# Kernel optimization log

Hardware: AMD Instinct MI355X
Metric: run time of the kernel (lower is better)

The kernel has to match this reference:

```python
import jax, jax.numpy as jnp
import numpy as np

N, E, G, L, D = 50000, 800000, 512, 3, 128
BN_EPS = 1e-5


def setup_inputs() -> dict:
    key = jax.random.key(0)
    ks = jax.random.split(key, 16)
    x = jax.random.normal(ks[0], (N, D), dtype=jnp.float32)
    edge_index = jax.random.randint(ks[1], (2, E), 0, N)
    batch = jnp.sort(jax.random.randint(ks[2], (N,), 0, G))
    W1 = jax.random.normal(ks[3], (L, D, D), dtype=jnp.float32) * 0.05
    b1 = jax.random.normal(ks[4], (L, D), dtype=jnp.float32) * 0.05
    gamma = jax.random.uniform(ks[5], (L, D), dtype=jnp.float32) + 0.5
    beta = jax.random.normal(ks[6], (L, D), dtype=jnp.float32) * 0.05
    running_mean = jax.random.normal(ks[7], (L, D), dtype=jnp.float32) * 0.1
    running_var = jax.random.uniform(ks[8], (L, D), dtype=jnp.float32) + 0.5
    W2 = jax.random.normal(ks[9], (L, D, D), dtype=jnp.float32) * 0.05
    b2 = jax.random.normal(ks[10], (L, D), dtype=jnp.float32) * 0.05
    lin1_W = jax.random.normal(ks[11], (L * D, L * D), dtype=jnp.float32) * 0.05
    lin1_b = jax.random.normal(ks[12], (L * D,), dtype=jnp.float32) * 0.05
    lin2_W = jax.random.normal(ks[13], (L * D, 10), dtype=jnp.float32) * 0.05
    lin2_b = jax.random.normal(ks[14], (10,), dtype=jnp.float32) * 0.05
    return {"x": x, "edge_index": edge_index, "batch": batch,
            "W1": W1, "b1": b1, "gamma": gamma, "beta": beta,
            "running_mean": running_mean, "running_var": running_var,
            "W2": W2, "b2": b2, "lin1_W": lin1_W, "lin1_b": lin1_b,
            "lin2_W": lin2_W, "lin2_b": lin2_b}


def _gin_layer(h, src, dst, W1, b1, gamma, beta, rm, rv, W2, b2):
    # GINConv (eps=0): MLP((1+eps)*x + sum_{j->i} x_j); aggregate src->dst
    agg = jax.ops.segment_sum(h[src], dst, num_segments=N)  # [N, D]
    z = (h + agg) @ W1 + b1
    # BatchNorm1d in eval mode (running stats)
    z = (z - rm) * (gamma / jnp.sqrt(rv + BN_EPS)) + beta
    z = jax.nn.relu(z)
    return jax.nn.relu(z @ W2 + b2)


def reference(x, edge_index, batch, W1, b1, gamma, beta, running_mean,
              running_var, W2, b2, lin1_W, lin1_b, lin2_W, lin2_b):
    src, dst = edge_index[0], edge_index[1]
    h = x
    pooled = []
    for i in range(L):
        h = _gin_layer(h, src, dst, W1[i], b1[i], gamma[i], beta[i],
                       running_mean[i], running_var[i], W2[i], b2[i])
        pooled.append(jax.ops.segment_sum(h, batch, num_segments=G))  # [G, D]
    g = jnp.concatenate(pooled, axis=1)  # [G, L*D]
    g = jax.nn.relu(g @ lin1_W + lin1_b)
    # dropout is identity in eval mode
    return g @ lin2_W + lin2_b  # [G, num_classes]
```

## Files before the change

### kernel.cpp

```cpp
#include <hip/hip_runtime.h>
#include <hip/hip_bf16.h>

#define D_FEAT 128
#define N_GRAPHS 512
#define N_LAYERS 3
#define POOL_DIM (N_LAYERS * D_FEAT)
#define N_CLASSES 10
#define BN_EPS 1e-5f
#define CAP 64
#define NBINS 8
#define SLABCAP 768


typedef __attribute__((ext_vector_type(8))) short bf16x8;
typedef __attribute__((ext_vector_type(8))) unsigned short ushort8;
typedef __attribute__((ext_vector_type(4))) float f32x4;

__device__ __forceinline__ unsigned short f2bf(float f) {
    unsigned u = __builtin_bit_cast(unsigned, f);
    u += 0x7FFFu + ((u >> 16) & 1u);
    return (unsigned short)(u >> 16);
}
__device__ __forceinline__ float bf2f(unsigned short h) {
    unsigned u = ((unsigned)h) << 16;
    return __builtin_bit_cast(float, u);
}
__device__ __forceinline__ float bf_lo(unsigned u) {
    return __builtin_bit_cast(float, u << 16);
}
__device__ __forceinline__ float bf_hi(unsigned u) {
    return __builtin_bit_cast(float, u & 0xffff0000u);
}

__global__ __launch_bounds__(256) void setup_kernel(
        const float* __restrict__ x, unsigned short* __restrict__ xb,
        const float* __restrict__ W1, const float* __restrict__ W2,
        unsigned short* __restrict__ Wt,
        const float* __restrict__ b1, const float* __restrict__ gamma,
        const float* __restrict__ beta, const float* __restrict__ rm,
        const float* __restrict__ rv, const float* __restrict__ b2,
        float* __restrict__ ea, float* __restrict__ eb,
        int* __restrict__ cursor, float* __restrict__ pooled,
        const int* __restrict__ ei, int2* __restrict__ pairs,
        int* __restrict__ cnts, int E,
        int N, int n4, int B0, int B1, int B2, int B3, int B4) {
    int b = blockIdx.x, tid = threadIdx.x;
    if (b < B0) {
        int i = b * 256 + tid;
        if (i < n4) {
            float4 v = ((const float4*)x)[i];
            ushort4 o;
            o.x = f2bf(v.x); o.y = f2bf(v.y); o.z = f2bf(v.z); o.w = f2bf(v.w);
            ((ushort4*)xb)[i] = o;
        }
    } else if (b < B1) {
        __shared__ float tile[64][65];
        int t = b - B0;
        int slot = t >> 2;
        int r0 = ((t >> 1) & 1) * 64;
        int c0 = (t & 1) * 64;
        int l = slot >> 1;
        const float* W = (slot & 1) ? W2 : W1;
        const float* Wb = W + (size_t)l * D_FEAT * D_FEAT;
        int rr = tid >> 2, cc4 = (tid & 3) * 16;
        #pragma unroll
        for (int j = 0; j < 16; ++j)
            tile[rr][cc4 + j] = Wb[(size_t)(r0 + rr) * D_FEAT + c0 + cc4 + j];
        __syncthreads();
        int nn = tid >> 2, kk4 = (tid & 3) * 16;
        unsigned short* Wo = Wt + (size_t)slot * D_FEAT * D_FEAT;
        #pragma unroll
        for (int j = 0; j < 16; ++j)
            Wo[(size_t)(c0 + nn) * D_FEAT + r0 + kk4 + j] = f2bf(tile[kk4 + j][nn]);
    } else if (b < B2) {
        int i = (b - B1) * 256 + tid;
        if (i < N_LAYERS * D_FEAT) {
            int l = i >> 7, c = i & 127;
            float s = gamma[i] * rsqrtf(rv[i] + BN_EPS);
            ea[(2 * l) * D_FEAT + c] = s;
            eb[(2 * l) * D_FEAT + c] = (b1[i] - rm[i]) * s + beta[i];
            ea[(2 * l + 1) * D_FEAT + c] = 1.0f;
            eb[(2 * l + 1) * D_FEAT + c] = b2[i];
        }
    } else if (b < B3) {
        int i = (b - B2) * 256 + tid;
        if (i < N) cursor[i] = 0;
    } else if (b < B4) {
        int i = (b - B3) * 256 + tid;
        if (i < N_GRAPHS * POOL_DIM) pooled[i] = 0.f;
    } else {
        __shared__ int loc[NBINS];
        int bb = b - B4;
        int per = (E + 255) / 256;
        int e0 = bb * per;
        int e1 = e0 + per; if (e1 > E) e1 = E;
        int span = (N + NBINS - 1) / NBINS;
        if (tid < NBINS) loc[tid] = 0;
        __syncthreads();
        for (int e = e0 + tid; e < e1; e += 256) {
            int dst = ei[E + e];
            int src = ei[e];
            int bin = dst / span;
            int p = atomicAdd(&loc[bin], 1);
            if (p < SLABCAP)
                pairs[((size_t)(bin * 256 + bb)) * SLABCAP + p] = make_int2(src, dst);
        }
        __syncthreads();
        if (tid < NBINS)
            cnts[tid * 256 + bb] = loc[tid];
    }
}

__global__ __launch_bounds__(256) void fill_v3(const int2* __restrict__ pairs,
                                               const int* __restrict__ cnts,
                                               int* __restrict__ cursor,
                                               int* __restrict__ bucket) {
    int r = blockIdx.x & 7;
    int chunk = blockIdx.x >> 3;
    #pragma unroll
    for (int s = 0; s < 4; ++s) {
        int blk = chunk * 4 + s;
        int cnt = cnts[r * 256 + blk];
        if (cnt > SLABCAP) cnt = SLABCAP;
        const int2* slab = pairs + (size_t)(r * 256 + blk) * SLABCAP;
        for (int p = threadIdx.x; p < cnt; p += 256) {
            int2 pr = slab[p];
            int pos = atomicAdd(&cursor[pr.y], 1);
            if (pos < CAP) bucket[(size_t)pr.y * CAP + pos] = pr.x;
        }
    }
}

__global__ __launch_bounds__(256) void agg_kernel(const unsigned short* __restrict__ hprev,
                                                  const int* __restrict__ deg,
                                                  const int* __restrict__ bucket,
                                                  unsigned short* __restrict__ y, int n) {
    int wave = threadIdx.x >> 6, lane = threadIdx.x & 63;
    int n0 = (blockIdx.x * 4 + wave) * 2;
    if (n0 >= n) return;
    int n1 = n0 + 1;
    bool v1 = (n1 < n);
    int d0 = deg[n0]; if (d0 > CAP) d0 = CAP;
    int d1 = v1 ? deg[n1] : 0; if (d1 > CAP) d1 = CAP;
    int grp = lane >> 4, sub = lane & 15;
    const uint4* hp = (const uint4*)hprev;

    int idx0 = bucket[(size_t)n0 * CAP + lane];
    int idx1 = v1 ? bucket[(size_t)n1 * CAP + lane] : 0;

    uint4 s0v = hp[(size_t)n0 * 16 + sub];
    uint4 s1v = v1 ? hp[(size_t)n1 * 16 + sub] : make_uint4(0u, 0u, 0u, 0u);

    float a0[8] = {0.f,0.f,0.f,0.f,0.f,0.f,0.f,0.f};
    float a1[8] = {0.f,0.f,0.f,0.f,0.f,0.f,0.f,0.f};
    int dmax = d0 > d1 ? d0 : d1;

    auto issue = [&](int t, bool (&p0)[4], bool (&p1)[4],
                     uint4 (&w0)[4], uint4 (&w1)[4]) {
        #pragma unroll
        for (int q = 0; q < 4; ++q) {
            int e = t + q * 4 + grp;
            int s0 = __shfl(idx0, e & 63);
            int s1 = __shfl(idx1, e & 63);
            p0[q] = e < d0;
            p1[q] = e < d1;
            int r0 = p0[q] ? s0 : n0;
            int r1 = p1[q] ? s1 : n0;
            w0[q] = hp[(size_t)r0 * 16 + sub];
            w1[q] = hp[(size_t)r1 * 16 + sub];
        }
    };
    auto accum = [&](bool (&p0)[4], bool (&p1)[4],
                     uint4 (&w0)[4], uint4 (&w1)[4]) {
        #pragma unroll
        for (int q = 0; q < 4; ++q) {
            if (p0[q]) {
                uint4 v = w0[q];
                a0[0] += bf_lo(v.x); a0[1] += bf_hi(v.x);
                a0[2] += bf_lo(v.y); a0[3] += bf_hi(v.y);
                a0[4] += bf_lo(v.z); a0[5] += bf_hi(v.z);
                a0[6] += bf_lo(v.w); a0[7] += bf_hi(v.w);
            }
            if (p1[q]) {
                uint4 v = w1[q];
                a1[0] += bf_lo(v.x); a1[1] += bf_hi(v.x);
                a1[2] += bf_lo(v.y); a1[3] += bf_hi(v.y);
                a1[4] += bf_lo(v.z); a1[5] += bf_hi(v.z);
                a1[6] += bf_lo(v.w); a1[7] += bf_hi(v.w);
            }
        }
    };

    if (dmax > 0) {
        bool cp0[4], cp1[4];
        uint4 cw0[4], cw1[4];
        issue(0, cp0, cp1, cw0, cw1);
        for (int t = 16; t < dmax; t += 16) {
            bool np0[4], np1[4];
            uint4 nw0[4], nw1[4];
            issue(t, np0, np1, nw0, nw1);
            accum(cp0, cp1, cw0, cw1);
            #pragma unroll
            for (int q = 0; q < 4; ++q) {
                cp0[q] = np0[q]; cp1[q] = np1[q];
                cw0[q] = nw0[q]; cw1[q] = nw1[q];
            }
        }
        accum(cp0, cp1, cw0, cw1);
    }

    #pragma unroll
    for (int j = 0; j < 8; ++j) {
        a0[j] += __shfl_xor(a0[j], 16);
        a0[j] += __shfl_xor(a0[j], 32);
        a1[j] += __shfl_xor(a1[j], 16);
        a1[j] += __shfl_xor(a1[j], 32);
    }

    a0[0] += bf_lo(s0v.x); a0[1] += bf_hi(s0v.x);
    a0[2] += bf_lo(s0v.y); a0[3] += bf_hi(s0v.y);
    a0[4] += bf_lo(s0v.z); a0[5] += bf_hi(s0v.z);
    a0[6] += bf_lo(s0v.w); a0[7] += bf_hi(s0v.w);
    if (v1) {
        a1[0] += bf_lo(s1v.x); a1[1] += bf_hi(s1v.x);
        a1[2] += bf_lo(s1v.y); a1[3] += bf_hi(s1v.y);
        a1[4] += bf_lo(s1v.z); a1[5] += bf_hi(s1v.z);
        a1[6] += bf_lo(s1v.w); a1[7] += bf_hi(s1v.w);
    }

    if (grp == 0) {
        uint4 o;
        o.x = (unsigned)f2bf(a0[0]) | ((unsigned)f2bf(a0[1]) << 16);
        o.y = (unsigned)f2bf(a0[2]) | ((unsigned)f2bf(a0[3]) << 16);
        o.z = (unsigned)f2bf(a0[4]) | ((unsigned)f2bf(a0[5]) << 16);
        o.w = (unsigned)f2bf(a0[6]) | ((unsigned)f2bf(a0[7]) << 16);
        ((uint4*)y)[(size_t)n0 * 16 + sub] = o;
        if (v1) {
            uint4 p;
            p.x = (unsigned)f2bf(a1[0]) | ((unsigned)f2bf(a1[1]) << 16);
            p.y = (unsigned)f2bf(a1[2]) | ((unsigned)f2bf(a1[3]) << 16);
            p.z = (unsigned)f2bf(a1[4]) | ((unsigned)f2bf(a1[5]) << 16);
            p.w = (unsigned)f2bf(a1[6]) | ((unsigned)f2bf(a1[7]) << 16);
            ((uint4*)y)[(size_t)n1 * 16 + sub] = p;
        }
    }
}

__global__ __launch_bounds__(256) void layer_fused(const unsigned short* __restrict__ A,
                                                   const unsigned short* __restrict__ Wt1,
                                                   const unsigned short* __restrict__ Wt2,
                                                   const float* __restrict__ ea1,
                                                   const float* __restrict__ eb1,
                                                   const float* __restrict__ ea2,
                                                   const float* __restrict__ eb2,
                                                   const int* __restrict__ batch,
                                                   float* __restrict__ pooled, int loff,
                                                   unsigned short* __restrict__ outh, int n) {
    __shared__ unsigned short As[64][136];
    __shared__ unsigned short Ws[128][136];
    __shared__ int bgsh[64];
    int tid = threadIdx.x;
    int row0 = blockIdx.x * 64;
    int wave = tid >> 6, lane = tid & 63;
    int m0 = wave * 16;
    int lrow = lane & 15, lq = lane >> 4;

    #pragma unroll
    for (int i = 0; i < 4; ++i) {
        int idx = tid + i * 256;
        int r = idx >> 4, c = (idx & 15) * 8;
        ushort8 v = (ushort8)0;
        if (row0 + r < n) v = *(const ushort8*)&A[(size_t)(row0 + r) * D_FEAT + c];
        *(ushort8*)&As[r][c] = v;
    }
    #pragma unroll
    for (int i = 0; i < 8; ++i) {
        int idx = tid + i * 256;
        int r = idx >> 4, c = (idx & 15) * 8;
        *(ushort8*)&Ws[r][c] = *(const ushort8*)&Wt1[(size_t)r * D_FEAT + c];
    }
    if (tid < 64)
        bgsh[tid] = (row0 + tid < n) ? batch[row0 + tid] : -1;

    ushort8 w2reg[8];
    #pragma unroll
    for (int i = 0; i < 8; ++i) {
        int idx = tid + i * 256;
        int r = idx >> 4, c = (idx & 15) * 8;
        w2reg[i] = *(const ushort8*)&Wt2[(size_t)r * D_FEAT + c];
    }
    __syncthreads();

    f32x4 acc[8] = {};
    #pragma unroll
    for (int t = 0; t < 4; ++t) {
        bf16x8 a = *(const bf16x8*)&As[m0 + lrow][t * 32 + lq * 8];
        #pragma unroll
        for (int nt = 0; nt < 8; ++nt) {
            bf16x8 b = *(const bf16x8*)&Ws[nt * 16 + lrow][t * 32 + lq * 8];
            acc[nt] = __builtin_amdgcn_mfma_f32_16x16x32_bf16(a, b, acc[nt], 0, 0, 0);
        }
    }
    __syncthreads();

    #pragma unroll
    for (int nt = 0; nt < 8; ++nt) {
        int col = nt * 16 + lrow;
        float al = ea1[col], be = eb1[col];
        #pragma unroll
        for (int r = 0; r < 4; ++r) {
            float v = fmaxf(fmaf(acc[nt][r], al, be), 0.f);
            As[m0 + lq * 4 + r][col] = f2bf(v);
        }
    }
    #pragma unroll
    for (int i = 0; i < 8; ++i) {
        int idx = tid + i * 256;
        int r = idx >> 4, c = (idx & 15) * 8;
        *(ushort8*)&Ws[r][c] = w2reg[i];
    }
    __syncthreads();

    f32x4 acc2[8] = {};
    #pragma unroll
    for (int t = 0; t < 4; ++t) {
        bf16x8 a = *(const bf16x8*)&As[m0 + lrow][t * 32 + lq * 8];
        #pragma unroll
        for (int nt = 0; nt < 8; ++nt) {
            bf16x8 b = *(const bf16x8*)&Ws[nt * 16 + lrow][t * 32 + lq * 8];
            acc2[nt] = __builtin_amdgcn_mfma_f32_16x16x32_bf16(a, b, acc2[nt], 0, 0, 0);
        }
    }

    if (outh) {
        #pragma unroll
        for (int nt = 0; nt < 8; ++nt) {
            int col = nt * 16 + lrow;
            float al = ea2[col], be = eb2[col];
            #pragma unroll
            for (int r = 0; r < 4; ++r) {
                int grow = row0 + m0 + lq * 4 + r;
                if (grow < n) {
                    float v = fmaxf(fmaf(acc2[nt][r], al, be), 0.f);
                    outh[(size_t)grow * D_FEAT + col] = f2bf(v);
                }
            }
        }
    }

    __syncthreads();
    float* Wsf = (float*)Ws;
    #pragma unroll
    for (int nt = 0; nt < 8; ++nt) {
        int col = nt * 16 + lrow;
        float al = ea2[col], be = eb2[col];
        #pragma unroll
        for (int r = 0; r < 4; ++r) {
            int lr = m0 + lq * 4 + r;
            float v = fmaxf(fmaf(acc2[nt][r], al, be), 0.f);
            Wsf[lr * 132 + col] = bf2f(f2bf(v));
        }
    }
    __syncthreads();

    int c = tid & 127, half = tid >> 7;
    int rbeg = half * 32, rend = rbeg + 32;
    int cur = -1; float sum = 0.f;
    for (int r = rbeg; r < rend; ++r) {
        int g = bgsh[r];
        if (g != cur) {
            if (cur >= 0) atomicAdd(&pooled[(size_t)cur * POOL_DIM + loff + c], sum);
            cur = g; sum = 0.f;
        }
        if (g >= 0) sum += Wsf[r * 132 + c];
    }
    if (cur >= 0) atomicAdd(&pooled[(size_t)cur * POOL_DIM + loff + c], sum);
}

__global__ __launch_bounds__(384) void fc1_kernel(const float* __restrict__ pooled,
                                                  const float* __restrict__ W1,
                                                  const float* __restrict__ b1v,
                                                  float* __restrict__ f1) {
    int j = threadIdx.x;
    int g0 = blockIdx.x * 4;
    const float* pr = pooled + (size_t)g0 * POOL_DIM;
    float bb = b1v[j];
    float s0 = bb, s1 = bb, s2 = bb, s3 = bb;
    for (int k0 = 0; k0 < POOL_DIM; k0 += 8) {
        float w[8];
        #pragma unroll
        for (int i = 0; i < 8; ++i)
            w[i] = W1[(size_t)(k0 + i) * POOL_DIM + j];
        #pragma unroll
        for (int i = 0; i < 8; ++i) {
            int k = k0 + i;
            s0 = fmaf(pr[k],                w[i], s0);
            s1 = fmaf(pr[POOL_DIM + k],     w[i], s1);
            s2 = fmaf(pr[2 * POOL_DIM + k], w[i], s2);
            s3 = fmaf(pr[3 * POOL_DIM + k], w[i], s3);
        }
    }
    f1[(size_t)(g0 + 0) * POOL_DIM + j] = fmaxf(s0, 0.f);
    f1[(size_t)(g0 + 1) * POOL_DIM + j] = fmaxf(s1, 0.f);
    f1[(size_t)(g0 + 2) * POOL_DIM + j] = fmaxf(s2, 0.f);
    f1[(size_t)(g0 + 3) * POOL_DIM + j] = fmaxf(s3, 0.f);
}

__global__ void fc2_kernel(const float* __restrict__ f1, const float* __restrict__ W,
                           const float* __restrict__ b, float* __restrict__ out) {
    int idx = blockIdx.x * 256 + threadIdx.x;
    if (idx >= N_GRAPHS * N_CLASSES) return;
    int r = idx / N_CLASSES, c = idx % N_CLASSES;
    float s = b[c];
    const float* prow = f1 + (size_t)r * POOL_DIM;
    for (int k = 0; k < POOL_DIM; ++k)
        s = fmaf(prow[k], W[(size_t)k * N_CLASSES + c], s);
    out[idx] = s;
}

extern "C" void kernel_launch(void* const* d_in, const int* in_sizes, int n_in,
                              void* d_out, int out_size, void* d_ws, size_t ws_size,
                              hipStream_t stream) {
    const float* x      = (const float*)d_in[0];
    const int*   ei     = (const int*)  d_in[1];
    const int*   batch  = (const int*)  d_in[2];
    const float* W1     = (const float*)d_in[3];
    const float* b1     = (const float*)d_in[4];
    const float* gamma  = (const float*)d_in[5];
    const float* beta   = (const float*)d_in[6];
    const float* rm     = (const float*)d_in[7];
    const float* rv     = (const float*)d_in[8];
    const float* W2     = (const float*)d_in[9];
    const float* b2     = (const float*)d_in[10];
    const float* lin1W  = (const float*)d_in[11];
    const float* lin1b  = (const float*)d_in[12];
    const float* lin2W  = (const float*)d_in[13];
    const float* lin2b  = (const float*)d_in[14];
    float* out = (float*)d_out;

    const int N = in_sizes[0] / D_FEAT;
    const int E = in_sizes[1] / 2;

    char* ws = (char*)d_ws;
    auto carve = [&](size_t bytes) {
        char* p = ws;
        ws += (bytes + 255) & ~(size_t)255;
        return p;
    };
    int*   cursor    = (int*)  carve((size_t)N * 4);
    int*   cnts      = (int*)  carve((size_t)NBINS * 256 * 4);
    int*   bucket    = (int*)  carve((size_t)N * CAP * 4);
    int2*  pairs     = (int2*) carve((size_t)NBINS * 256 * SLABCAP * 8);
    float* ea        = (float*)carve((size_t)2 * N_LAYERS * D_FEAT * 4);
    float* eb        = (float*)carve((size_t)2 * N_LAYERS * D_FEAT * 4);
    unsigned short* Wt   = (unsigned short*)carve((size_t)2 * N_LAYERS * D_FEAT * D_FEAT * 2);
    unsigned short* xb   = (unsigned short*)carve((size_t)N * D_FEAT * 2);
    unsigned short* ybuf = (unsigned short*)carve((size_t)N * D_FEAT * 2);
    unsigned short* hbuf = (unsigned short*)carve((size_t)N * D_FEAT * 2);
    float* pooled    = (float*)carve((size_t)N_GRAPHS * POOL_DIM * 4);
    float* f1buf     = (float*)carve((size_t)N_GRAPHS * POOL_DIM * 4);

    const int n4 = N * D_FEAT / 4;
    const int B0 = (n4 + 255) / 256;
    const int B1 = B0 + 24;
    const int B2 = B1 + 2;
    const int B3 = B2 + (N + 255) / 256;
    const int B4 = B3 + (N_GRAPHS * POOL_DIM + 255) / 256;
    const int B5 = B4 + 256;

    setup_kernel<<<B5, 256, 0, stream>>>(x, xb, W1, W2, Wt, b1, gamma, beta,
                                         rm, rv, b2, ea, eb, cursor, pooled,
                                         ei, pairs, cnts, E,
                                         N, n4, B0, B1, B2, B3, B4);
    fill_v3<<<8 * 64, 256, 0, stream>>>(pairs, cnts, cursor, bucket);

    const unsigned short* hprev = xb;
    for (int l = 0; l < N_LAYERS; ++l) {
        agg_kernel<<<(N + 7) / 8, 256, 0, stream>>>(hprev, cursor, bucket, ybuf, N);
        unsigned short* outh = (l == N_LAYERS - 1) ? nullptr : hbuf;
        layer_fused<<<(N + 63) / 64, 256, 0, stream>>>(ybuf,
                      Wt + (size_t)(2 * l) * D_FEAT * D_FEAT,
                      Wt + (size_t)(2 * l + 1) * D_FEAT * D_FEAT,
                      ea + (size_t)(2 * l) * D_FEAT,
                      eb + (size_t)(2 * l) * D_FEAT,
                      ea + (size_t)(2 * l + 1) * D_FEAT,
                      eb + (size_t)(2 * l + 1) * D_FEAT,
                      batch, pooled, l * D_FEAT, outh, N);
        hprev = hbuf;
    }
    fc1_kernel<<<N_GRAPHS / 4, 384, 0, stream>>>(pooled, lin1W, lin1b, f1buf);
    fc2_kernel<<<(N_GRAPHS * N_CLASSES + 255) / 256, 256, 0, stream>>>(f1buf, lin2W, lin2b, out);
}
```

Before: 352.8 us.

## Double per-block rows in fused layer MLP and fuse fc1/fc2 head kernels

The fused layer kernel now processes 128 rows per block, with each wave computing two 16-row MFMA subtiles. This amortizes loading both 128x128 weight matrices into LDS over twice as many rows, and it uses a single raw shared buffer for the A tile, the W tile and the fp32 pooling scratch. Separately, fc1 and fc2 are merged into one head kernel that keeps the hidden activations in shared memory, removing one launch and a global round trip. In exchange, accumulator registers per thread double and the block count halves, which may lower occupancy and parallelism.

```diff
diff --git a/kernel.cpp b/kernel.cpp
--- a/kernel.cpp
+++ b/kernel.cpp
@@ -256,17 +256,18 @@
                                                    const int* __restrict__ batch,
                                                    float* __restrict__ pooled, int loff,
                                                    unsigned short* __restrict__ outh, int n) {
-    __shared__ unsigned short As[64][136];
-    __shared__ unsigned short Ws[128][136];
-    __shared__ int bgsh[64];
+    __shared__ __align__(16) char shraw[2 * 128 * 136 * 2];
+    unsigned short (*As)[136] = (unsigned short (*)[136])shraw;
+    unsigned short (*Ws)[136] = (unsigned short (*)[136])(shraw + 128 * 136 * 2);
+    __shared__ int bgsh[128];
     int tid = threadIdx.x;
-    int row0 = blockIdx.x * 64;
+    int row0 = blockIdx.x * 128;
     int wave = tid >> 6, lane = tid & 63;
-    int m0 = wave * 16;
+    int m0 = wave * 32;
     int lrow = lane & 15, lq = lane >> 4;
 
     #pragma unroll
-    for (int i = 0; i < 4; ++i) {
+    for (int i = 0; i < 8; ++i) {
         int idx = tid + i * 256;
         int r = idx >> 4, c = (idx & 15) * 8;
         ushort8 v = (ushort8)0;
@@ -279,7 +280,7 @@
         int r = idx >> 4, c = (idx & 15) * 8;
         *(ushort8*)&Ws[r][c] = *(const ushort8*)&Wt1[(size_t)r * D_FEAT + c];
     }
-    if (tid < 64)
+    if (tid < 128)
         bgsh[tid] = (row0 + tid < n) ? batch[row0 + tid] : -1;
 
     ushort8 w2reg[8];
@@ -291,26 +292,32 @@
     }
     __syncthreads();
 
-    f32x4 acc[8] = {};
-    #pragma unroll
-    for (int t = 0; t < 4; ++t) {
-        bf16x8 a = *(const bf16x8*)&As[m0 + lrow][t * 32 + lq * 8];
+    f32x4 acc[2][8] = {};
+    #pragma unroll
+    for (int s = 0; s < 2; ++s) {
+        #pragma unroll
+        for (int t = 0; t < 4; ++t) {
+            bf16x8 a = *(const bf16x8*)&As[m0 + s * 16 + lrow][t * 32 + lq * 8];
+            #pragma unroll
+            for (int nt = 0; nt < 8; ++nt) {
+                bf16x8 b = *(const bf16x8*)&Ws[nt * 16 + lrow][t * 32 + lq * 8];
+                acc[s][nt] = __builtin_amdgcn_mfma_f32_16x16x32_bf16(a, b, acc[s][nt], 0, 0, 0);
+            }
+        }
+    }
+    __syncthreads();
+
+    #pragma unroll
+    for (int s = 0; s < 2; ++s) {
         #pragma unroll
         for (int nt = 0; nt < 8; ++nt) {
-            bf16x8 b = *(const bf16x8*)&Ws[nt * 16 + lrow][t * 32 + lq * 8];
-            acc[nt] = __builtin_amdgcn_mfma_f32_16x16x32_bf16(a, b, acc[nt], 0, 0, 0);
-        }
-    }
-    __syncthreads();
-
-    #pragma unroll
-    for (int nt = 0; nt < 8; ++nt) {
-        int col = nt * 16 + lrow;
-        float al = ea1[col], be = eb1[col];
-        #pragma unroll
-        for (int r = 0; r < 4; ++r) {
-            float v = fmaxf(fmaf(acc[nt][r], al, be), 0.f);
-            As[m0 + lq * 4 + r][col] = f2bf(v);
+            int col = nt * 16 + lrow;
+            float al = ea1[col], be = eb1[col];
+            #pragma unroll
+            for (int r = 0; r < 4; ++r) {
+                float v = fmaxf(fmaf(acc[s][nt][r], al, be), 0.f);
+                As[m0 + s * 16 + lq * 4 + r][col] = f2bf(v);
+            }
         }
     }
     #pragma unroll
@@ -321,50 +328,59 @@
     }
     __syncthreads();
 
-    f32x4 acc2[8] = {};
-    #pragma unroll
-    for (int t = 0; t < 4; ++t) {
-        bf16x8 a = *(const bf16x8*)&As[m0 + lrow][t * 32 + lq * 8];
-        #pragma unroll
-        for (int nt = 0; nt < 8; ++nt) {
-            bf16x8 b = *(const bf16x8*)&Ws[nt * 16 + lrow][t * 32 + lq * 8];
-            acc2[nt] = __builtin_amdgcn_mfma_f32_16x16x32_bf16(a, b, acc2[nt], 0, 0, 0);
+    f32x4 acc2[2][8] = {};
+    #pragma unroll
+    for (int s = 0; s < 2; ++s) {
+        #pragma unroll
+        for (int t = 0; t < 4; ++t) {
+            bf16x8 a = *(const bf16x8*)&As[m0 + s * 16 + lrow][t * 32 + lq * 8];
+            #pragma unroll
+            for (int nt = 0; nt < 8; ++nt) {
+                bf16x8 b = *(const bf16x8*)&Ws[nt * 16 + lrow][t * 32 + lq * 8];
+                acc2[s][nt] = __builtin_amdgcn_mfma_f32_16x16x32_bf16(a, b, acc2[s][nt], 0, 0, 0);
+            }
         }
     }
 
     if (outh) {
+        #pragma unroll
+        for (int s = 0; s < 2; ++s) {
+            #pragma unroll
+            for (int nt = 0; nt < 8; ++nt) {
+                int col = nt * 16 + lrow;
+                float al = ea2[col], be = eb2[col];
+                #pragma unroll
+                for (int r = 0; r < 4; ++r) {
+                    int grow = row0 + m0 + s * 16 + lq * 4 + r;
+                    if (grow < n) {
+                        float v = fmaxf(fmaf(acc2[s][nt][r], al, be), 0.f);
+                        outh[(size_t)grow * D_FEAT + col] = f2bf(v);
+                    }
+                }
+            }
+        }
+    }
+
+    __syncthreads();
+    float (*P)[132] = (float (*)[132])shraw;
+    #pragma unroll
+    for (int s = 0; s < 2; ++s) {
         #pragma unroll
         for (int nt = 0; nt < 8; ++nt) {
             int col = nt * 16 + lrow;
             float al = ea2[col], be = eb2[col];
             #pragma unroll
             for (int r = 0; r < 4; ++r) {
-                int grow = row0 + m0 + lq * 4 + r;
-                if (grow < n) {
-                    float v = fmaxf(fmaf(acc2[nt][r], al, be), 0.f);
-                    outh[(size_t)grow * D_FEAT + col] = f2bf(v);
-                }
-            }
-        }
-    }
-
+                int lr = m0 + s * 16 + lq * 4 + r;
+                float v = fmaxf(fmaf(acc2[s][nt][r], al, be), 0.f);
+                P[lr][col] = bf2f(f2bf(v));
+            }
+        }
+    }
     __syncthreads();
-    float* Wsf = (float*)Ws;
-    #pragma unroll
-    for (int nt = 0; nt < 8; ++nt) {
-        int col = nt * 16 + lrow;
-        float al = ea2[col], be = eb2[col];
-        #pragma unroll
-        for (int r = 0; r < 4; ++r) {
-            int lr = m0 + lq * 4 + r;
-            float v = fmaxf(fmaf(acc2[nt][r], al, be), 0.f);
-            Wsf[lr * 132 + col] = bf2f(f2bf(v));
-        }
-    }
-    __syncthreads();
 
     int c = tid & 127, half = tid >> 7;
-    int rbeg = half * 32, rend = rbeg + 32;
+    int rbeg = half * 64, rend = rbeg + 64;
     int cur = -1; float sum = 0.f;
     for (int r = rbeg; r < rend; ++r) {
         int g = bgsh[r];
@@ -372,15 +388,18 @@
             if (cur >= 0) atomicAdd(&pooled[(size_t)cur * POOL_DIM + loff + c], sum);
             cur = g; sum = 0.f;
         }
-        if (g >= 0) sum += Wsf[r * 132 + c];
+        if (g >= 0) sum += P[r][c];
     }
     if (cur >= 0) atomicAdd(&pooled[(size_t)cur * POOL_DIM + loff + c], sum);
 }
 
-__global__ __launch_bounds__(384) void fc1_kernel(const float* __restrict__ pooled,
-                                                  const float* __restrict__ W1,
-                                                  const float* __restrict__ b1v,
-                                                  float* __restrict__ f1) {
+__global__ __launch_bounds__(384) void head_kernel(const float* __restrict__ pooled,
+                                                   const float* __restrict__ W1,
+                                                   const float* __restrict__ b1v,
+                                                   const float* __restrict__ W2,
+                                                   const float* __restrict__ b2v,
+                                                   float* __restrict__ out) {
+    __shared__ float f1[4][POOL_DIM];
     int j = threadIdx.x;
     int g0 = blockIdx.x * 4;
     const float* pr = pooled + (size_t)g0 * POOL_DIM;
@@ -400,22 +419,18 @@
             s3 = fmaf(pr[3 * POOL_DIM + k], w[i], s3);
         }
     }
-    f1[(size_t)(g0 + 0) * POOL_DIM + j] = fmaxf(s0, 0.f);
-    f1[(size_t)(g0 + 1) * POOL_DIM + j] = fmaxf(s1, 0.f);
-    f1[(size_t)(g0 + 2) * POOL_DIM + j] = fmaxf(s2, 0.f);
-    f1[(size_t)(g0 + 3) * POOL_DIM + j] = fmaxf(s3, 0.f);
-}
-
-__global__ void fc2_kernel(const float* __restrict__ f1, const float* __restrict__ W,
-                           const float* __restrict__ b, float* __restrict__ out) {
-    int idx = blockIdx.x * 256 + threadIdx.x;
-    if (idx >= N_GRAPHS * N_CLASSES) return;
-    int r = idx / N_CLASSES, c = idx % N_CLASSES;
-    float s = b[c];
-    const float* prow = f1 + (size_t)r * POOL_DIM;
-    for (int k = 0; k < POOL_DIM; ++k)
-        s = fmaf(prow[k], W[(size_t)k * N_CLASSES + c], s);
-    out[idx] = s;
+    f1[0][j] = fmaxf(s0, 0.f);
+    f1[1][j] = fmaxf(s1, 0.f);
+    f1[2][j] = fmaxf(s2, 0.f);
+    f1[3][j] = fmaxf(s3, 0.f);
+    __syncthreads();
+    if (j < 4 * N_CLASSES) {
+        int g = j / N_CLASSES, c = j % N_CLASSES;
+        float s = b2v[c];
+        for (int k = 0; k < POOL_DIM; ++k)
+            s = fmaf(f1[g][k], W2[(size_t)k * N_CLASSES + c], s);
+        out[(size_t)(g0 + g) * N_CLASSES + c] = s;
+    }
 }
 
 extern "C" void kernel_launch(void* const* d_in, const int* in_sizes, int n_in,
@@ -458,7 +473,6 @@
     unsigned short* ybuf = (unsigned short*)carve((size_t)N * D_FEAT * 2);
     unsigned short* hbuf = (unsigned short*)carve((size_t)N * D_FEAT * 2);
     float* pooled    = (float*)carve((size_t)N_GRAPHS * POOL_DIM * 4);
-    float* f1buf     = (float*)carve((size_t)N_GRAPHS * POOL_DIM * 4);
 
     const int n4 = N * D_FEAT / 4;
     const int B0 = (n4 + 255) / 256;
@@ -478,7 +492,7 @@
     for (int l = 0; l < N_LAYERS; ++l) {
         agg_kernel<<<(N + 7) / 8, 256, 0, stream>>>(hprev, cursor, bucket, ybuf, N);
         unsigned short* outh = (l == N_LAYERS - 1) ? nullptr : hbuf;
-        layer_fused<<<(N + 63) / 64, 256, 0, stream>>>(ybuf,
+        layer_fused<<<(N + 127) / 128, 256, 0, stream>>>(ybuf,
                       Wt + (size_t)(2 * l) * D_FEAT * D_FEAT,
                       Wt + (size_t)(2 * l + 1) * D_FEAT * D_FEAT,
                       ea + (size_t)(2 * l) * D_FEAT,
@@ -488,6 +502,5 @@
                       batch, pooled, l * D_FEAT, outh, N);
         hprev = hbuf;
     }
-    fc1_kernel<<<N_GRAPHS / 4, 384, 0, stream>>>(pooled, lin1W, lin1b, f1buf);
-    fc2_kernel<<<(N_GRAPHS * N_CLASSES + 255) / 256, 256, 0, stream>>>(f1buf, lin2W, lin2b, out);
-}
+    head_kernel<<<N_GRAPHS / 4, 384, 0, stream>>>(pooled, lin1W, lin1b, lin2W, lin2b, out);
+}
```

Measured after the change: 391.9 us. 1.11x slower.
